# Optimization experiments

Measured on AMD Instinct MI355X. Metric: run time of the kernel, lower is better.

The kernel has to match this reference:

```python
import jax, jax.numpy as jnp
import numpy as np

HIDDEN = 1024
HEADS = 16
HEAD = HIDDEN // HEADS


def _ternary_weight(key, shape):
    g = jax.random.normal(key, shape, dtype=jnp.float32)
    return jnp.where(jnp.abs(g) < 0.6, 0.0, jnp.sign(g)).astype(jnp.float32)


def setup_inputs() -> dict:
    key = jax.random.key(0)
    ks = jax.random.split(key, 10)
    x = jax.random.normal(ks[0], (2, 2048, HIDDEN), dtype=jnp.float32)
    d = {"x": x}
    names = ["q", "k", "v", "o"]
    for i, n in enumerate(names):
        d[f"w_{n}"] = _ternary_weight(ks[1 + i], (HIDDEN, HIDDEN))
        d[f"s_{n}"] = jnp.float32(0.02)  # per-layer dequant scale
        d[f"b_{n}"] = jax.random.normal(ks[5 + i], (HIDDEN,), dtype=jnp.float32) * 0.02
    return d


def _tlin(x, w, s, b):
    # dequantized ternary linear: x @ (s * w).T + b
    return jnp.einsum("bsh,oh->bso", x, w) * s + b


def reference(x, w_q, s_q, b_q, w_k, s_k, b_k, w_v, s_v, b_v, w_o, s_o, b_o):
    B, S, H = x.shape
    def split_heads(t):
        return t.reshape(B, S, HEADS, HEAD).transpose(0, 2, 1, 3)  # [B, nH, S, hd]
    q = split_heads(_tlin(x, w_q, s_q, b_q))
    k = split_heads(_tlin(x, w_k, s_k, b_k))
    v = split_heads(_tlin(x, w_v, s_v, b_v))
    scores = jnp.einsum("bhqd,bhkd->bhqk", q, k) / jnp.sqrt(jnp.float32(HEAD))
    attn = jax.nn.softmax(scores, axis=-1)
    ctx = jnp.einsum("bhqk,bhkd->bhqd", attn, v)
    ctx = ctx.transpose(0, 2, 1, 3).reshape(B, S, H)
    return _tlin(ctx, w_o, s_o, b_o)
```

## Files before the change

kernel.cpp:

```cpp
#include <hip/hip_runtime.h>
#include <hip/hip_bf16.h>

typedef unsigned short u16;
typedef __bf16 bf16x8 __attribute__((ext_vector_type(8)));
typedef __bf16 bf16x4 __attribute__((ext_vector_type(4)));
typedef float f32x4 __attribute__((ext_vector_type(4)));
typedef unsigned short u16x8 __attribute__((ext_vector_type(8)));

__device__ inline u16 f2bf(float f) {
    union { float f; unsigned u; } v; v.f = f;
    unsigned r = v.u + 0x7fffu + ((v.u >> 16) & 1u);
    return (u16)(r >> 16);
}

__global__ void convert_kernel(const float* __restrict__ x,
                               const float* __restrict__ wq, const float* __restrict__ wk,
                               const float* __restrict__ wv, const float* __restrict__ wo,
                               u16* __restrict__ dst) {
    long g = (long)blockIdx.x * blockDim.x + threadIdx.x;
    const float* src; long base;
    const long GX = 1048576, GW = 262144;
    if (g < GX)            { src = x;  base = 0; }
    else if (g < GX + GW)  { src = wq; base = GX; }
    else if (g < GX + 2*GW){ src = wk; base = GX + GW; }
    else if (g < GX + 3*GW){ src = wv; base = GX + 2*GW; }
    else                   { src = wo; base = GX + 3*GW; }
    long rel = g - base;
    float4 v = reinterpret_cast<const float4*>(src)[rel];
    ushort4 o;
    o.x = f2bf(v.x); o.y = f2bf(v.y); o.z = f2bf(v.z); o.w = f2bf(v.w);
    reinterpret_cast<ushort4*>(dst)[g] = o;
}

__device__ inline void gemm_mainloop(const u16* __restrict__ A, const u16* __restrict__ W,
                                     int t0, int n0, u16* As, u16* Bs, f32x4 acc[4][4]) {
    const int tid = threadIdx.x;
    const int wid = tid >> 6, lane = tid & 63, quad = lane >> 4, ln = lane & 15;
    const int wm = wid >> 1, wn = wid & 1;
#pragma unroll
    for (int im = 0; im < 4; im++)
#pragma unroll
        for (int in = 0; in < 4; in++) acc[im][in] = (f32x4){0.f, 0.f, 0.f, 0.f};

    for (int k0 = 0; k0 < 1024; k0 += 64) {
#pragma unroll
        for (int i = 0; i < 4; i++) {
            int chunk = wid * 4 + i;
            int b = chunk * 1024 + lane * 16;
            int row = b >> 7;
            int cb = (b & 127) ^ ((row & 7) << 4);
            const u16* gA = A + (long)(t0 + row) * 1024 + k0 + (cb >> 1);
            const u16* gB = W + (long)(n0 + row) * 1024 + k0 + (cb >> 1);
            __builtin_amdgcn_global_load_lds((const __attribute__((address_space(1))) void*)gA,
                                             (__attribute__((address_space(3))) void*)(As + chunk * 512),
                                             16, 0, 0);
            __builtin_amdgcn_global_load_lds((const __attribute__((address_space(1))) void*)gB,
                                             (__attribute__((address_space(3))) void*)(Bs + chunk * 512),
                                             16, 0, 0);
        }
        __syncthreads();
#pragma unroll
        for (int ks = 0; ks < 2; ks++) {
            bf16x8 af[4], bfr[4];
#pragma unroll
            for (int im = 0; im < 4; im++) {
                int r = wm * 64 + im * 16 + ln;
                int byt = (r * 128 + ks * 64 + quad * 16) ^ ((r & 7) << 4);
                af[im] = *reinterpret_cast<const bf16x8*>((const char*)As + byt);
            }
#pragma unroll
            for (int in = 0; in < 4; in++) {
                int r = wn * 64 + in * 16 + ln;
                int byt = (r * 128 + ks * 64 + quad * 16) ^ ((r & 7) << 4);
                bfr[in] = *reinterpret_cast<const bf16x8*>((const char*)Bs + byt);
            }
#pragma unroll
            for (int im = 0; im < 4; im++)
#pragma unroll
                for (int in = 0; in < 4; in++)
                    acc[im][in] = __builtin_amdgcn_mfma_f32_16x16x32_bf16(af[im], bfr[in], acc[im][in], 0, 0, 0);
        }
        __syncthreads();
    }
}

__global__ void qkv_gemm(const u16* __restrict__ x_bf,
                         const u16* __restrict__ wq, const u16* __restrict__ wk, const u16* __restrict__ wv,
                         const float* __restrict__ sq, const float* __restrict__ sk, const float* __restrict__ sv,
                         const float* __restrict__ bq, const float* __restrict__ bk, const float* __restrict__ bv,
                         u16* __restrict__ q_ws, u16* __restrict__ k_ws, u16* __restrict__ v_ws) {
    __shared__ __align__(16) u16 As[128 * 64];
    __shared__ __align__(16) u16 Bs[128 * 64];
    const int z = blockIdx.z;
    const u16* W   = (z == 0) ? wq : (z == 1) ? wk : wv;
    const float* sp = (z == 0) ? sq : (z == 1) ? sk : sv;
    const float* bp = (z == 0) ? bq : (z == 1) ? bk : bv;
    u16* dst = (z == 0) ? q_ws : (z == 1) ? k_ws : v_ws;
    const float extra = (z == 0) ? 0.125f * 1.44269504088896f : 1.0f;
    const int t0 = blockIdx.x * 128, n0 = blockIdx.y * 128;

    f32x4 acc[4][4];
    gemm_mainloop(x_bf, W, t0, n0, As, Bs, acc);

    const int tid = threadIdx.x;
    const int wid = tid >> 6, lane = tid & 63, quad = lane >> 4, ln = lane & 15;
    const int wm = wid >> 1, wn = wid & 1;
    const float s = sp[0] * extra;
#pragma unroll
    for (int in = 0; in < 4; in++) {
        int col = n0 + wn * 64 + in * 16 + ln;
        float bias = bp[col] * extra;
        int h = col >> 6, d = col & 63;
#pragma unroll
        for (int im = 0; im < 4; im++) {
            int rbase = t0 + wm * 64 + im * 16 + quad * 4;
#pragma unroll
            for (int j = 0; j < 4; j++) {
                int t = rbase + j;
                int b = t >> 11, ss = t & 2047;
                int bh = b * 16 + h;
                float val = acc[im][in][j] * s + bias;
                long idx = (z < 2) ? ((long)(bh * 2048 + ss) * 64 + d)
                                   : ((long)(bh * 64 + d) * 2048 + ss);
                dst[idx] = f2bf(val);
            }
        }
    }
}

#define LDP 72

__global__ void __launch_bounds__(512)
attn_kernel(const u16* __restrict__ q_ws, const u16* __restrict__ k_ws,
            const u16* __restrict__ v_ws, u16* __restrict__ ctx) {
    __shared__ u16 Kt[64 * LDP];
    __shared__ u16 Vt[64 * LDP];
    __shared__ u16 Pt[128 * LDP];

    const int tid = threadIdx.x;
    const int wid = tid >> 6, lane = tid & 63, quad = lane >> 4, ln = lane & 15;
    const int bh = blockIdx.y;
    const int q0 = blockIdx.x * 128;
    const u16* qbase = q_ws + (long)bh * 2048 * 64;
    const u16* kbase = k_ws + (long)bh * 2048 * 64;
    const u16* vbase = v_ws + (long)bh * 64 * 2048;

    bf16x8 aq[2];
#pragma unroll
    for (int ks = 0; ks < 2; ks++)
        aq[ks] = *reinterpret_cast<const bf16x8*>(
            qbase + (long)(q0 + wid * 16 + ln) * 64 + ks * 32 + quad * 8);

    f32x4 acc_o[4];
    float lsum = 0.f;
#pragma unroll
    for (int dt = 0; dt < 4; dt++) acc_o[dt] = (f32x4){0.f, 0.f, 0.f, 0.f};

    const int srow = tid >> 3, skc = tid & 7;
    u16x8 kreg = *reinterpret_cast<const u16x8*>(kbase + (long)srow * 64 + skc * 8);
    u16x8 vreg = *reinterpret_cast<const u16x8*>(vbase + (long)srow * 2048 + skc * 8);

    for (int kt = 0; kt < 2048; kt += 64) {
        *reinterpret_cast<u16x8*>(Kt + srow * LDP + skc * 8) = kreg;
        *reinterpret_cast<u16x8*>(Vt + srow * LDP + skc * 8) = vreg;
        if (kt + 64 < 2048) {
            kreg = *reinterpret_cast<const u16x8*>(kbase + (long)(kt + 64 + srow) * 64 + skc * 8);
            vreg = *reinterpret_cast<const u16x8*>(vbase + (long)srow * 2048 + (kt + 64) + skc * 8);
        }
        __syncthreads();

#pragma unroll
        for (int k8 = 0; k8 < 4; k8++) {
            bf16x8 a0 = *reinterpret_cast<const bf16x8*>(Kt + (k8 * 16 + ln) * LDP + quad * 8);
            bf16x8 a1 = *reinterpret_cast<const bf16x8*>(Kt + (k8 * 16 + ln) * LDP + 32 + quad * 8);
            f32x4 t = (f32x4){0.f, 0.f, 0.f, 0.f};
            t = __builtin_amdgcn_mfma_f32_16x16x32_bf16(a0, aq[0], t, 0, 0, 0);
            t = __builtin_amdgcn_mfma_f32_16x16x32_bf16(a1, aq[1], t, 0, 0, 0);
            __bf16 p0 = (__bf16)__builtin_amdgcn_exp2f(t[0]);
            __bf16 p1 = (__bf16)__builtin_amdgcn_exp2f(t[1]);
            __bf16 p2 = (__bf16)__builtin_amdgcn_exp2f(t[2]);
            __bf16 p3 = (__bf16)__builtin_amdgcn_exp2f(t[3]);
            lsum += (float)p0 + (float)p1 + (float)p2 + (float)p3;
            *reinterpret_cast<bf16x4*>(Pt + (wid * 16 + ln) * LDP + k8 * 16 + quad * 4)
                = (bf16x4){p0, p1, p2, p3};
        }

#pragma unroll
        for (int step = 0; step < 2; step++) {
            bf16x8 ap = *reinterpret_cast<const bf16x8*>(
                Pt + (wid * 16 + ln) * LDP + step * 32 + quad * 8);
#pragma unroll
            for (int dt = 0; dt < 4; dt++) {
                bf16x8 bv = *reinterpret_cast<const bf16x8*>(
                    Vt + (dt * 16 + ln) * LDP + step * 32 + quad * 8);
                acc_o[dt] = __builtin_amdgcn_mfma_f32_16x16x32_bf16(ap, bv, acc_o[dt], 0, 0, 0);
            }
        }
        __syncthreads();
    }

    const int b = bh >> 4, h = bh & 15;
    float lt = lsum;
    lt += __shfl_xor(lt, 16, 64);
    lt += __shfl_xor(lt, 32, 64);
#pragma unroll
    for (int j = 0; j < 4; j++) {
        float rinv = 1.0f / __shfl(lt, quad * 4 + j, 64);
        int t = b * 2048 + q0 + wid * 16 + quad * 4 + j;
#pragma unroll
        for (int dt = 0; dt < 4; dt++) {
            float val = acc_o[dt][j] * rinv;
            ctx[(long)t * 1024 + h * 64 + dt * 16 + ln] = f2bf(val);
        }
    }
}

__global__ void o_gemm(const u16* __restrict__ ctx, const u16* __restrict__ wo,
                       const float* __restrict__ so, const float* __restrict__ bo,
                       float* __restrict__ out) {
    __shared__ __align__(16) u16 As[128 * 64];
    __shared__ __align__(16) u16 Bs[128 * 64];
    const int t0 = blockIdx.x * 128, n0 = blockIdx.y * 128;
    f32x4 acc[4][4];
    gemm_mainloop(ctx, wo, t0, n0, As, Bs, acc);

    const int tid = threadIdx.x;
    const int wid = tid >> 6, lane = tid & 63, quad = lane >> 4, ln = lane & 15;
    const int wm = wid >> 1, wn = wid & 1;
    const float s = so[0];
#pragma unroll
    for (int in = 0; in < 4; in++) {
        int col = n0 + wn * 64 + in * 16 + ln;
        float bias = bo[col];
#pragma unroll
        for (int im = 0; im < 4; im++) {
            int rbase = t0 + wm * 64 + im * 16 + quad * 4;
#pragma unroll
            for (int j = 0; j < 4; j++)
                out[(long)(rbase + j) * 1024 + col] = acc[im][in][j] * s + bias;
        }
    }
}

extern "C" void kernel_launch(void* const* d_in, const int* in_sizes, int n_in,
                              void* d_out, int out_size, void* d_ws, size_t ws_size,
                              hipStream_t stream) {
    const float* x   = (const float*)d_in[0];
    const float* w_q = (const float*)d_in[1];
    const float* s_q = (const float*)d_in[2];
    const float* b_q = (const float*)d_in[3];
    const float* w_k = (const float*)d_in[4];
    const float* s_k = (const float*)d_in[5];
    const float* b_k = (const float*)d_in[6];
    const float* w_v = (const float*)d_in[7];
    const float* s_v = (const float*)d_in[8];
    const float* b_v = (const float*)d_in[9];
    const float* w_o = (const float*)d_in[10];
    const float* s_o = (const float*)d_in[11];
    const float* b_o = (const float*)d_in[12];

    if (ws_size < (size_t)50331648) return;

    u16* ws     = (u16*)d_ws;
    u16* x_bf   = ws;
    u16* wq_bf  = x_bf  + 4194304;
    u16* wk_bf  = wq_bf + 1048576;
    u16* wv_bf  = wk_bf + 1048576;
    u16* wo_bf  = wv_bf + 1048576;
    u16* q_ws   = wo_bf + 1048576;
    u16* k_ws   = q_ws  + 4194304;
    u16* v_ws   = k_ws  + 4194304;
    u16* ctx_ws = v_ws  + 4194304;

    convert_kernel<<<dim3(8192), dim3(256), 0, stream>>>(x, w_q, w_k, w_v, w_o, ws);
    qkv_gemm<<<dim3(32, 8, 3), dim3(256), 0, stream>>>(x_bf, wq_bf, wk_bf, wv_bf,
                                                       s_q, s_k, s_v, b_q, b_k, b_v,
                                                       q_ws, k_ws, v_ws);
    attn_kernel<<<dim3(16, 32), dim3(512), 0, stream>>>(q_ws, k_ws, v_ws, ctx_ws);
    o_gemm<<<dim3(32, 8), dim3(256), 0, stream>>>(ctx_ws, wo_bf, s_o, b_o, (float*)d_out);
}
```

Measured before the change: 207.7 us.

## Double-buffer K/V tiles via direct global-to-LDS loads and shrink o_gemm N-tile

The attention kernel now streams K and V tiles into double-buffered, XOR-swizzled LDS with global_load_lds, replacing register staging. This removes one barrier per iteration and the register-to-LDS copies, so loads of the next tile overlap compute on the current one. The o_gemm is templated to a 128x64 tile, doubling its grid from 256 to 512 blocks to fill more CUs on this small GEMM. In exchange, LDS use per attention block grows and the o_gemm reloads A tiles more often.

```diff
diff --git a/kernel.cpp b/kernel.cpp
--- a/kernel.cpp
+++ b/kernel.cpp
@@ -32,36 +32,38 @@
     reinterpret_cast<ushort4*>(dst)[g] = o;
 }
 
+template<int NFR>
 __device__ inline void gemm_mainloop(const u16* __restrict__ A, const u16* __restrict__ W,
-                                     int t0, int n0, u16* As, u16* Bs, f32x4 acc[4][4]) {
+                                     int t0, int n0, u16* As, u16* Bs,
+                                     f32x4 (&acc)[4][NFR]) {
     const int tid = threadIdx.x;
     const int wid = tid >> 6, lane = tid & 63, quad = lane >> 4, ln = lane & 15;
     const int wm = wid >> 1, wn = wid & 1;
+    const int PER = 4 + NFR;
 #pragma unroll
     for (int im = 0; im < 4; im++)
 #pragma unroll
-        for (int in = 0; in < 4; in++) acc[im][in] = (f32x4){0.f, 0.f, 0.f, 0.f};
+        for (int in = 0; in < NFR; in++) acc[im][in] = (f32x4){0.f, 0.f, 0.f, 0.f};
 
     for (int k0 = 0; k0 < 1024; k0 += 64) {
 #pragma unroll
-        for (int i = 0; i < 4; i++) {
-            int chunk = wid * 4 + i;
+        for (int i = 0; i < PER; i++) {
+            int c = wid * PER + i;
+            int chunk = (c < 16) ? c : c - 16;
             int b = chunk * 1024 + lane * 16;
             int row = b >> 7;
             int cb = (b & 127) ^ ((row & 7) << 4);
-            const u16* gA = A + (long)(t0 + row) * 1024 + k0 + (cb >> 1);
-            const u16* gB = W + (long)(n0 + row) * 1024 + k0 + (cb >> 1);
-            __builtin_amdgcn_global_load_lds((const __attribute__((address_space(1))) void*)gA,
-                                             (__attribute__((address_space(3))) void*)(As + chunk * 512),
+            const u16* g = (c < 16) ? A + (long)(t0 + row) * 1024 + k0 + (cb >> 1)
+                                    : W + (long)(n0 + row) * 1024 + k0 + (cb >> 1);
+            u16* d = ((c < 16) ? As : Bs) + chunk * 512;
+            __builtin_amdgcn_global_load_lds((const __attribute__((address_space(1))) void*)g,
+                                             (__attribute__((address_space(3))) void*)d,
                                              16, 0, 0);
-            __builtin_amdgcn_global_load_lds((const __attribute__((address_space(1))) void*)gB,
-                                             (__attribute__((address_space(3))) void*)(Bs + chunk * 512),
-                                             16, 0, 0);
         }
         __syncthreads();
 #pragma unroll
         for (int ks = 0; ks < 2; ks++) {
-            bf16x8 af[4], bfr[4];
+            bf16x8 af[4], bfr[NFR];
 #pragma unroll
             for (int im = 0; im < 4; im++) {
                 int r = wm * 64 + im * 16 + ln;
@@ -69,15 +71,15 @@
                 af[im] = *reinterpret_cast<const bf16x8*>((const char*)As + byt);
             }
 #pragma unroll
-            for (int in = 0; in < 4; in++) {
-                int r = wn * 64 + in * 16 + ln;
+            for (int in = 0; in < NFR; in++) {
+                int r = wn * (NFR * 16) + in * 16 + ln;
                 int byt = (r * 128 + ks * 64 + quad * 16) ^ ((r & 7) << 4);
                 bfr[in] = *reinterpret_cast<const bf16x8*>((const char*)Bs + byt);
             }
 #pragma unroll
             for (int im = 0; im < 4; im++)
 #pragma unroll
-                for (int in = 0; in < 4; in++)
+                for (int in = 0; in < NFR; in++)
                     acc[im][in] = __builtin_amdgcn_mfma_f32_16x16x32_bf16(af[im], bfr[in], acc[im][in], 0, 0, 0);
         }
         __syncthreads();
@@ -100,7 +102,7 @@
     const int t0 = blockIdx.x * 128, n0 = blockIdx.y * 128;
 
     f32x4 acc[4][4];
-    gemm_mainloop(x_bf, W, t0, n0, As, Bs, acc);
+    gemm_mainloop<4>(x_bf, W, t0, n0, As, Bs, acc);
 
     const int tid = threadIdx.x;
     const int wid = tid >> 6, lane = tid & 63, quad = lane >> 4, ln = lane & 15;
@@ -133,8 +135,8 @@
 __global__ void __launch_bounds__(512)
 attn_kernel(const u16* __restrict__ q_ws, const u16* __restrict__ k_ws,
             const u16* __restrict__ v_ws, u16* __restrict__ ctx) {
-    __shared__ u16 Kt[64 * LDP];
-    __shared__ u16 Vt[64 * LDP];
+    __shared__ __align__(16) u16 Kb[2][4096];
+    __shared__ __align__(16) u16 Vb[2][4096];
     __shared__ u16 Pt[128 * LDP];
 
     const int tid = threadIdx.x;
@@ -145,6 +147,10 @@
     const u16* kbase = k_ws + (long)bh * 2048 * 64;
     const u16* vbase = v_ws + (long)bh * 64 * 2048;
 
+    const int srow = wid * 8 + (lane >> 3);
+    const int sel  = 8 * ((lane & 7) ^ ((lane >> 3) & 7));
+    const int xr = (ln & 7) << 4;
+
     bf16x8 aq[2];
 #pragma unroll
     for (int ks = 0; ks < 2; ks++)
@@ -156,23 +162,39 @@
 #pragma unroll
     for (int dt = 0; dt < 4; dt++) acc_o[dt] = (f32x4){0.f, 0.f, 0.f, 0.f};
 
-    const int srow = tid >> 3, skc = tid & 7;
-    u16x8 kreg = *reinterpret_cast<const u16x8*>(kbase + (long)srow * 64 + skc * 8);
-    u16x8 vreg = *reinterpret_cast<const u16x8*>(vbase + (long)srow * 2048 + skc * 8);
-
+    {
+        const u16* gk = kbase + (long)srow * 64 + sel;
+        const u16* gv = vbase + (long)srow * 2048 + sel;
+        __builtin_amdgcn_global_load_lds((const __attribute__((address_space(1))) void*)gk,
+                                         (__attribute__((address_space(3))) void*)(&Kb[0][wid * 512]),
+                                         16, 0, 0);
+        __builtin_amdgcn_global_load_lds((const __attribute__((address_space(1))) void*)gv,
+                                         (__attribute__((address_space(3))) void*)(&Vb[0][wid * 512]),
+                                         16, 0, 0);
+    }
+    __syncthreads();
+
+    int cur = 0;
     for (int kt = 0; kt < 2048; kt += 64) {
-        *reinterpret_cast<u16x8*>(Kt + srow * LDP + skc * 8) = kreg;
-        *reinterpret_cast<u16x8*>(Vt + srow * LDP + skc * 8) = vreg;
         if (kt + 64 < 2048) {
-            kreg = *reinterpret_cast<const u16x8*>(kbase + (long)(kt + 64 + srow) * 64 + skc * 8);
-            vreg = *reinterpret_cast<const u16x8*>(vbase + (long)srow * 2048 + (kt + 64) + skc * 8);
-        }
-        __syncthreads();
+            const u16* gk = kbase + (long)(kt + 64 + srow) * 64 + sel;
+            const u16* gv = vbase + (long)srow * 2048 + (kt + 64) + sel;
+            __builtin_amdgcn_global_load_lds((const __attribute__((address_space(1))) void*)gk,
+                                             (__attribute__((address_space(3))) void*)(&Kb[cur ^ 1][wid * 512]),
+                                             16, 0, 0);
+            __builtin_amdgcn_global_load_lds((const __attribute__((address_space(1))) void*)gv,
+                                             (__attribute__((address_space(3))) void*)(&Vb[cur ^ 1][wid * 512]),
+                                             16, 0, 0);
+        }
+        const char* Kc = (const char*)(&Kb[cur][0]);
+        const char* Vc = (const char*)(&Vb[cur][0]);
 
 #pragma unroll
         for (int k8 = 0; k8 < 4; k8++) {
-            bf16x8 a0 = *reinterpret_cast<const bf16x8*>(Kt + (k8 * 16 + ln) * LDP + quad * 8);
-            bf16x8 a1 = *reinterpret_cast<const bf16x8*>(Kt + (k8 * 16 + ln) * LDP + 32 + quad * 8);
+            bf16x8 a0 = *reinterpret_cast<const bf16x8*>(
+                Kc + (k8 * 16 + ln) * 128 + ((quad * 16) ^ xr));
+            bf16x8 a1 = *reinterpret_cast<const bf16x8*>(
+                Kc + (k8 * 16 + ln) * 128 + ((64 + quad * 16) ^ xr));
             f32x4 t = (f32x4){0.f, 0.f, 0.f, 0.f};
             t = __builtin_amdgcn_mfma_f32_16x16x32_bf16(a0, aq[0], t, 0, 0, 0);
             t = __builtin_amdgcn_mfma_f32_16x16x32_bf16(a1, aq[1], t, 0, 0, 0);
@@ -192,11 +214,12 @@
 #pragma unroll
             for (int dt = 0; dt < 4; dt++) {
                 bf16x8 bv = *reinterpret_cast<const bf16x8*>(
-                    Vt + (dt * 16 + ln) * LDP + step * 32 + quad * 8);
+                    Vc + (dt * 16 + ln) * 128 + ((step * 64 + quad * 16) ^ xr));
                 acc_o[dt] = __builtin_amdgcn_mfma_f32_16x16x32_bf16(ap, bv, acc_o[dt], 0, 0, 0);
             }
         }
         __syncthreads();
+        cur ^= 1;
     }
 
     const int b = bh >> 4, h = bh & 15;
@@ -219,18 +242,18 @@
                        const float* __restrict__ so, const float* __restrict__ bo,
                        float* __restrict__ out) {
     __shared__ __align__(16) u16 As[128 * 64];
-    __shared__ __align__(16) u16 Bs[128 * 64];
-    const int t0 = blockIdx.x * 128, n0 = blockIdx.y * 128;
-    f32x4 acc[4][4];
-    gemm_mainloop(ctx, wo, t0, n0, As, Bs, acc);
+    __shared__ __align__(16) u16 Bs[64 * 64];
+    const int t0 = blockIdx.x * 128, n0 = blockIdx.y * 64;
+    f32x4 acc[4][2];
+    gemm_mainloop<2>(ctx, wo, t0, n0, As, Bs, acc);
 
     const int tid = threadIdx.x;
     const int wid = tid >> 6, lane = tid & 63, quad = lane >> 4, ln = lane & 15;
     const int wm = wid >> 1, wn = wid & 1;
     const float s = so[0];
 #pragma unroll
-    for (int in = 0; in < 4; in++) {
-        int col = n0 + wn * 64 + in * 16 + ln;
+    for (int in = 0; in < 2; in++) {
+        int col = n0 + wn * 32 + in * 16 + ln;
         float bias = bo[col];
 #pragma unroll
         for (int im = 0; im < 4; im++) {
@@ -277,5 +300,5 @@
                                                        s_q, s_k, s_v, b_q, b_k, b_v,
                                                        q_ws, k_ws, v_ws);
     attn_kernel<<<dim3(16, 32), dim3(512), 0, stream>>>(q_ws, k_ws, v_ws, ctx_ws);
-    o_gemm<<<dim3(32, 8), dim3(256), 0, stream>>>(ctx_ws, wo_bf, s_o, b_o, (float*)d_out);
-}
+    o_gemm<<<dim3(32, 16), dim3(256), 0, stream>>>(ctx_ws, wo_bf, s_o, b_o, (float*)d_out);
+}
```

Result: slower. 222.8 us (+7.3%).

## Double-buffer K/V tiles via direct global-to-LDS loads with XOR swizzle

Applied to the files above, without the earlier changes.

Replaces the register-staged K/V tile loads in the attention kernel with direct global_load_lds transfers into double-buffered shared memory. An XOR swizzle on the 16-byte chunk index replaces row padding to avoid bank conflicts. s_setprio is raised around the MFMA groups. The aim is to overlap the next tile's load with compute and cut the register round trip and one barrier per iteration. It relies on the asynchronous LDS writes being complete at the end-of-loop barrier without an explicit vmcnt wait, which is a correctness risk.

```diff
diff --git a/kernel.cpp b/kernel.cpp
--- a/kernel.cpp
+++ b/kernel.cpp
@@ -133,8 +133,8 @@
 __global__ void __launch_bounds__(512)
 attn_kernel(const u16* __restrict__ q_ws, const u16* __restrict__ k_ws,
             const u16* __restrict__ v_ws, u16* __restrict__ ctx) {
-    __shared__ u16 Kt[64 * LDP];
-    __shared__ u16 Vt[64 * LDP];
+    __shared__ __align__(16) u16 Kb[2][4096];
+    __shared__ __align__(16) u16 Vb[2][4096];
     __shared__ u16 Pt[128 * LDP];
 
     const int tid = threadIdx.x;
@@ -145,6 +145,10 @@
     const u16* kbase = k_ws + (long)bh * 2048 * 64;
     const u16* vbase = v_ws + (long)bh * 64 * 2048;
 
+    const int srow = wid * 8 + (lane >> 3);
+    const int sel  = 8 * ((lane & 7) ^ ((lane >> 3) & 7));
+    const int xr = (ln & 7) << 4;
+
     bf16x8 aq[2];
 #pragma unroll
     for (int ks = 0; ks < 2; ks++)
@@ -156,26 +160,43 @@
 #pragma unroll
     for (int dt = 0; dt < 4; dt++) acc_o[dt] = (f32x4){0.f, 0.f, 0.f, 0.f};
 
-    const int srow = tid >> 3, skc = tid & 7;
-    u16x8 kreg = *reinterpret_cast<const u16x8*>(kbase + (long)srow * 64 + skc * 8);
-    u16x8 vreg = *reinterpret_cast<const u16x8*>(vbase + (long)srow * 2048 + skc * 8);
-
+    const u16* kp = kbase + (long)srow * 64 + sel;
+    const u16* vp = vbase + (long)srow * 2048 + sel;
+
+    __builtin_amdgcn_global_load_lds((const __attribute__((address_space(1))) void*)kp,
+                                     (__attribute__((address_space(3))) void*)(&Kb[0][wid * 512]),
+                                     16, 0, 0);
+    __builtin_amdgcn_global_load_lds((const __attribute__((address_space(1))) void*)vp,
+                                     (__attribute__((address_space(3))) void*)(&Vb[0][wid * 512]),
+                                     16, 0, 0);
+    kp += 4096; vp += 64;
+    __syncthreads();
+
+    int cur = 0;
     for (int kt = 0; kt < 2048; kt += 64) {
-        *reinterpret_cast<u16x8*>(Kt + srow * LDP + skc * 8) = kreg;
-        *reinterpret_cast<u16x8*>(Vt + srow * LDP + skc * 8) = vreg;
         if (kt + 64 < 2048) {
-            kreg = *reinterpret_cast<const u16x8*>(kbase + (long)(kt + 64 + srow) * 64 + skc * 8);
-            vreg = *reinterpret_cast<const u16x8*>(vbase + (long)srow * 2048 + (kt + 64) + skc * 8);
-        }
-        __syncthreads();
+            __builtin_amdgcn_global_load_lds((const __attribute__((address_space(1))) void*)kp,
+                                             (__attribute__((address_space(3))) void*)(&Kb[cur ^ 1][wid * 512]),
+                                             16, 0, 0);
+            __builtin_amdgcn_global_load_lds((const __attribute__((address_space(1))) void*)vp,
+                                             (__attribute__((address_space(3))) void*)(&Vb[cur ^ 1][wid * 512]),
+                                             16, 0, 0);
+            kp += 4096; vp += 64;
+        }
+        const char* Kc = (const char*)(&Kb[cur][0]);
+        const char* Vc = (const char*)(&Vb[cur][0]);
 
 #pragma unroll
         for (int k8 = 0; k8 < 4; k8++) {
-            bf16x8 a0 = *reinterpret_cast<const bf16x8*>(Kt + (k8 * 16 + ln) * LDP + quad * 8);
-            bf16x8 a1 = *reinterpret_cast<const bf16x8*>(Kt + (k8 * 16 + ln) * LDP + 32 + quad * 8);
+            bf16x8 a0 = *reinterpret_cast<const bf16x8*>(
+                Kc + (k8 * 16 + ln) * 128 + ((quad * 16) ^ xr));
+            bf16x8 a1 = *reinterpret_cast<const bf16x8*>(
+                Kc + (k8 * 16 + ln) * 128 + ((64 + quad * 16) ^ xr));
             f32x4 t = (f32x4){0.f, 0.f, 0.f, 0.f};
+            __builtin_amdgcn_s_setprio(1);
             t = __builtin_amdgcn_mfma_f32_16x16x32_bf16(a0, aq[0], t, 0, 0, 0);
             t = __builtin_amdgcn_mfma_f32_16x16x32_bf16(a1, aq[1], t, 0, 0, 0);
+            __builtin_amdgcn_s_setprio(0);
             __bf16 p0 = (__bf16)__builtin_amdgcn_exp2f(t[0]);
             __bf16 p1 = (__bf16)__builtin_amdgcn_exp2f(t[1]);
             __bf16 p2 = (__bf16)__builtin_amdgcn_exp2f(t[2]);
@@ -189,14 +210,23 @@
         for (int step = 0; step < 2; step++) {
             bf16x8 ap = *reinterpret_cast<const bf16x8*>(
                 Pt + (wid * 16 + ln) * LDP + step * 32 + quad * 8);
-#pragma unroll
-            for (int dt = 0; dt < 4; dt++) {
-                bf16x8 bv = *reinterpret_cast<const bf16x8*>(
-                    Vt + (dt * 16 + ln) * LDP + step * 32 + quad * 8);
-                acc_o[dt] = __builtin_amdgcn_mfma_f32_16x16x32_bf16(ap, bv, acc_o[dt], 0, 0, 0);
-            }
+            bf16x8 bv0 = *reinterpret_cast<const bf16x8*>(
+                Vc + (0 * 16 + ln) * 128 + ((step * 64 + quad * 16) ^ xr));
+            bf16x8 bv1 = *reinterpret_cast<const bf16x8*>(
+                Vc + (1 * 16 + ln) * 128 + ((step * 64 + quad * 16) ^ xr));
+            bf16x8 bv2 = *reinterpret_cast<const bf16x8*>(
+                Vc + (2 * 16 + ln) * 128 + ((step * 64 + quad * 16) ^ xr));
+            bf16x8 bv3 = *reinterpret_cast<const bf16x8*>(
+                Vc + (3 * 16 + ln) * 128 + ((step * 64 + quad * 16) ^ xr));
+            __builtin_amdgcn_s_setprio(1);
+            acc_o[0] = __builtin_amdgcn_mfma_f32_16x16x32_bf16(ap, bv0, acc_o[0], 0, 0, 0);
+            acc_o[1] = __builtin_amdgcn_mfma_f32_16x16x32_bf16(ap, bv1, acc_o[1], 0, 0, 0);
+            acc_o[2] = __builtin_amdgcn_mfma_f32_16x16x32_bf16(ap, bv2, acc_o[2], 0, 0, 0);
+            acc_o[3] = __builtin_amdgcn_mfma_f32_16x16x32_bf16(ap, bv3, acc_o[3], 0, 0, 0);
+            __builtin_amdgcn_s_setprio(0);
         }
         __syncthreads();
+        cur ^= 1;
     }
 
     const int b = bh >> 4, h = bh & 15;
```

New measurement: 204.0 us. About the same (-1.8%).
